# Performance work log

Measured on AMD Instinct MI355X. Metric: run time of the kernel, lower is better.

Reference implementation:

```python
import jax, jax.numpy as jnp
import numpy as np

EPS = 0.01      # label smoothing eps
LAM = 0.5       # SuperLoss lam
ALPHA = 0.25    # FocalLoss alpha
GAMMA = 2.0     # FocalLoss gamma


def lambertw_principal(y, iters=20):
    """Real principal-branch Lambert W for y >= -1/e, via Halley iterations.
    Replaces the scipy.special.lambertw CPU round-trip with on-device math."""
    y = jnp.maximum(y, -jnp.exp(-1.0) + 1e-7)  # clamp to domain of W0
    # init: branch-point series near -1/e, log1p-based elsewhere
    p = jnp.sqrt(2.0 * (jnp.e * y + 1.0))
    w_bp = -1.0 + p - p * p / 3.0
    w = jnp.where(y < 0.0, w_bp, jnp.log1p(y))

    def body(w, _):
        ew = jnp.exp(w)
        f = w * ew - y
        w1 = w + 1.0
        w_next = w - f / (ew * w1 - (w + 2.0) * f / (2.0 * w1))
        return w_next, None

    w, _ = jax.lax.scan(body, w, None, length=iters)
    return w


def setup_inputs() -> dict:
    key = jax.random.key(0)
    k1, k2 = jax.random.split(key)
    B, C = 2048, 50257
    output = jax.random.normal(k1, (B, C), dtype=jnp.float32)
    target = jax.random.randint(k2, (B,), 0, C, dtype=jnp.int64)
    return {"output": output, "target": target}


def reference(output, target):
    B, c = output.shape
    # label-smoothing uniform term: mean over batch of -sum(log_softmax)
    log_preds = jax.nn.log_softmax(output, axis=-1)          # [B, C]
    loss = (-log_preds.sum(axis=-1)).mean()                  # scalar

    # FocalLoss(Superloss=True) applied to log_preds (CE re-applies log_softmax,
    # idempotent on log_preds but kept for fidelity)
    lp2 = jax.nn.log_softmax(log_preds, axis=-1)
    ce = -jnp.take_along_axis(lp2, target[:, None], axis=-1)[:, 0]  # [B]
    pt = jnp.exp(-ce)
    focal = ALPHA * (1.0 - pt) ** GAMMA * ce                 # [B]

    # SuperLoss: sigma computed from detached loss (stop_gradient)
    tau = jnp.log(jnp.float32(c))                            # C == classes
    l_det = jax.lax.stop_gradient(focal)
    cl_score = l_det - tau
    y_ = 0.5 * jnp.maximum(-2.0 / jnp.e, cl_score / LAM)
    sigma = jnp.exp(-lambertw_principal(y_))                 # [B]
    sl = (focal - tau) * sigma + LAM * jnp.log(sigma) ** 2
    sl_mean = sl.mean()

    loss_cls = loss * EPS / c + (1.0 - EPS) * sl_mean
    return loss_cls, jnp.exp(sl_mean)
```

## Files before the change

### kernel.cpp

```cpp
#include <hip/hip_runtime.h>
#include <hip/hip_bf16.h>
#include <math.h>


#define EPS_LS 0.01
#define LAM 0.5
#define ALPHA 0.25

typedef float vf4 __attribute__((ext_vector_type(4)));

__global__ __launch_bounds__(256) void
row_kernel(const float* __restrict__ x, float4* __restrict__ ws, int C) {
    const int row = blockIdx.x;
    const int tid = threadIdx.x;
    const float* xr = x + (size_t)row * (size_t)C;

    float s0 = 0.0f, s1 = 0.0f, s2 = 0.0f, s3 = 0.0f;
    float t0 = 0.0f, t1 = 0.0f, t2 = 0.0f, t3 = 0.0f;

    const int mis = (int)(((size_t)row * (size_t)C) & 3);
    const int pre = (4 - mis) & 3;
    if (tid < pre) {
        float v = xr[tid];
        s0 = __expf(v); t0 = v;
    }
    const int nvec = (C - pre) >> 2;
    const vf4* xv = reinterpret_cast<const vf4*>(xr + pre);

    int i = tid;
    for (; i + 768 < nvec; i += 1024) {
        vf4 v0 = __builtin_nontemporal_load(&xv[i]);
        vf4 v1 = __builtin_nontemporal_load(&xv[i + 256]);
        vf4 v2 = __builtin_nontemporal_load(&xv[i + 512]);
        vf4 v3 = __builtin_nontemporal_load(&xv[i + 768]);
        s0 += (__expf(v0.x) + __expf(v0.y)) + (__expf(v0.z) + __expf(v0.w));
        t0 += (v0.x + v0.y) + (v0.z + v0.w);
        s1 += (__expf(v1.x) + __expf(v1.y)) + (__expf(v1.z) + __expf(v1.w));
        t1 += (v1.x + v1.y) + (v1.z + v1.w);
        s2 += (__expf(v2.x) + __expf(v2.y)) + (__expf(v2.z) + __expf(v2.w));
        t2 += (v2.x + v2.y) + (v2.z + v2.w);
        s3 += (__expf(v3.x) + __expf(v3.y)) + (__expf(v3.z) + __expf(v3.w));
        t3 += (v3.x + v3.y) + (v3.z + v3.w);
    }
    for (; i < nvec; i += 256) {
        vf4 v0 = __builtin_nontemporal_load(&xv[i]);
        s0 += (__expf(v0.x) + __expf(v0.y)) + (__expf(v0.z) + __expf(v0.w));
        t0 += (v0.x + v0.y) + (v0.z + v0.w);
    }
    const int done = pre + (nvec << 2);
    const int rem = C - done;
    if (tid < rem) {
        float v = xr[done + tid];
        s0 += __expf(v); t0 += v;
    }

    float S = (s0 + s1) + (s2 + s3);
    float T = (t0 + t1) + (t2 + t3);

    for (int off = 32; off > 0; off >>= 1) {
        S += __shfl_down(S, off, 64);
        T += __shfl_down(T, off, 64);
    }

    __shared__ float sh_s[4], sh_t[4];
    const int wave = tid >> 6, lane = tid & 63;
    if (lane == 0) { sh_s[wave] = S; sh_t[wave] = T; }
    __syncthreads();

    if (tid == 0) {
        float Sa = ((sh_s[0] + sh_s[1]) + (sh_s[2] + sh_s[3]));
        float Ta = ((sh_t[0] + sh_t[1]) + (sh_t[2] + sh_t[3]));
        ws[row] = make_float4(0.0f, Sa, Ta, 0.0f);
    }
}

__global__ __launch_bounds__(256) void
mid_kernel(const float4* __restrict__ ws, const float* __restrict__ x,
           const int* __restrict__ tgt, double2* __restrict__ part,
           int B, int C) {
    __shared__ double shA[256], shB[256];
    const int tid = threadIdx.x;
    const int row = blockIdx.x * 256 + tid;
    const double tau = log((double)C);
    const double Econst = 2.718281828459045235360287;

    double sl = 0.0, loss = 0.0;
    if (row < B) {
        float4 r = ws[row];
        const double M = (double)r.x;
        const double lse = log((double)r.y);
        const double SX = (double)r.z;
        const double xt = (double)x[(size_t)row * (size_t)C + tgt[row]];
        const double ce = M + lse - xt;
        const double pt = exp(-ce);
        const double omp = 1.0 - pt;
        const double focal = ALPHA * omp * omp * ce;
        const double cl = focal - tau;
        double y_ = 0.5 * fmax(-2.0 / Econst, cl / LAM);
        double y  = fmax(y_, -exp(-1.0) + 1e-7);
        double p  = sqrt(2.0 * (Econst * y + 1.0));
        double w  = (y < 0.0) ? (-1.0 + p - p * p / 3.0) : log1p(y);
        for (int it = 0; it < 20; ++it) {
            double ew = exp(w);
            double f  = w * ew - y;
            double w1 = w + 1.0;
            w = w - f / (ew * w1 - (w + 2.0) * f / (2.0 * w1));
        }
        const double sigma = exp(-w);
        const double lw = log(sigma);
        sl   = cl * sigma + LAM * lw * lw;
        loss = (double)C * (M + lse) - SX;
    }
    shA[tid] = sl; shB[tid] = loss;
    __syncthreads();
    for (int off = 128; off > 0; off >>= 1) {
        if (tid < off) { shA[tid] += shA[tid + off]; shB[tid] += shB[tid + off]; }
        __syncthreads();
    }
    if (tid == 0) part[blockIdx.x] = make_double2(shA[0], shB[0]);
}

__global__ void
final_kernel(const double2* __restrict__ part, float* __restrict__ out,
             int npart, int B, int C) {
    if (threadIdx.x != 0) return;
    double sl_sum = 0.0, loss_sum = 0.0;
    for (int i = 0; i < npart; ++i) { sl_sum += part[i].x; loss_sum += part[i].y; }
    const double sl_mean = sl_sum / (double)B;
    const double loss    = loss_sum / (double)B;
    const double loss_cls = loss * (EPS_LS / (double)C) + (1.0 - EPS_LS) * sl_mean;
    out[0] = (float)loss_cls;
    out[1] = (float)exp(sl_mean);
}

extern "C" void kernel_launch(void* const* d_in, const int* in_sizes, int n_in,
                              void* d_out, int out_size, void* d_ws, size_t ws_size,
                              hipStream_t stream) {
    const float* x   = (const float*)d_in[0];
    const int*   tgt = (const int*)d_in[1];
    float* out = (float*)d_out;
    float4* ws = (float4*)d_ws;

    const int B = in_sizes[1];
    const int C = in_sizes[0] / B;

    const int nmid = (B + 255) / 256;
    double2* part = reinterpret_cast<double2*>((char*)d_ws + (size_t)B * 16);

    row_kernel<<<B, 256, 0, stream>>>(x, ws, C);
    mid_kernel<<<nmid, 256, 0, stream>>>(ws, x, tgt, part, B, C);
    final_kernel<<<1, 64, 0, stream>>>(part, out, nmid, B, C);
}
```

Measured before the change: 492.0 us.

## Fuse row, per-row loss and final reduction into one kernel via last-block counter

```diff
diff --git a/kernel.cpp b/kernel.cpp
--- a/kernel.cpp
+++ b/kernel.cpp
@@ -9,11 +9,20 @@
 
 typedef float vf4 __attribute__((ext_vector_type(4)));
 
+__global__ void init_kernel(unsigned int* __restrict__ counter) {
+    *counter = 0u;
+}
+
 __global__ __launch_bounds__(256) void
-row_kernel(const float* __restrict__ x, float4* __restrict__ ws, int C) {
+fused_kernel(const float* __restrict__ x, const int* __restrict__ tgt,
+             double2* __restrict__ part, unsigned int* __restrict__ counter,
+             float* __restrict__ out, int B, int C) {
     const int row = blockIdx.x;
     const int tid = threadIdx.x;
     const float* xr = x + (size_t)row * (size_t)C;
+
+    float xt_f = 0.0f;
+    if (tid == 0) xt_f = xr[tgt[row]];
 
     float s0 = 0.0f, s1 = 0.0f, s2 = 0.0f, s3 = 0.0f;
     float t0 = 0.0f, t1 = 0.0f, t2 = 0.0f, t3 = 0.0f;
@@ -67,30 +76,17 @@
     if (lane == 0) { sh_s[wave] = S; sh_t[wave] = T; }
     __syncthreads();
 
+    __shared__ unsigned int lastflag;
     if (tid == 0) {
-        float Sa = ((sh_s[0] + sh_s[1]) + (sh_s[2] + sh_s[3]));
-        float Ta = ((sh_t[0] + sh_t[1]) + (sh_t[2] + sh_t[3]));
-        ws[row] = make_float4(0.0f, Sa, Ta, 0.0f);
-    }
-}
+        const float Sa = ((sh_s[0] + sh_s[1]) + (sh_s[2] + sh_s[3]));
+        const float Ta = ((sh_t[0] + sh_t[1]) + (sh_t[2] + sh_t[3]));
 
-__global__ __launch_bounds__(256) void
-mid_kernel(const float4* __restrict__ ws, const float* __restrict__ x,
-           const int* __restrict__ tgt, double2* __restrict__ part,
-           int B, int C) {
-    __shared__ double shA[256], shB[256];
-    const int tid = threadIdx.x;
-    const int row = blockIdx.x * 256 + tid;
-    const double tau = log((double)C);
-    const double Econst = 2.718281828459045235360287;
-
-    double sl = 0.0, loss = 0.0;
-    if (row < B) {
-        float4 r = ws[row];
-        const double M = (double)r.x;
-        const double lse = log((double)r.y);
-        const double SX = (double)r.z;
-        const double xt = (double)x[(size_t)row * (size_t)C + tgt[row]];
+        const double tau = log((double)C);
+        const double Econst = 2.718281828459045235360287;
+        const double M = 0.0;
+        const double lse = log((double)Sa);
+        const double SX = (double)Ta;
+        const double xt = (double)xt_f;
         const double ce = M + lse - xt;
         const double pt = exp(-ce);
         const double omp = 1.0 - pt;
@@ -108,29 +104,38 @@
         }
         const double sigma = exp(-w);
         const double lw = log(sigma);
-        sl   = cl * sigma + LAM * lw * lw;
-        loss = (double)C * (M + lse) - SX;
+        const double sl   = cl * sigma + LAM * lw * lw;
+        const double loss = (double)C * (M + lse) - SX;
+
+        part[row] = make_double2(sl, loss);
+        __threadfence();
+        unsigned int old = atomicAdd(counter, 1u);
+        lastflag = (old == (unsigned int)gridDim.x - 1u) ? 1u : 0u;
     }
-    shA[tid] = sl; shB[tid] = loss;
     __syncthreads();
-    for (int off = 128; off > 0; off >>= 1) {
-        if (tid < off) { shA[tid] += shA[tid + off]; shB[tid] += shB[tid + off]; }
+
+    if (lastflag) {
+        __threadfence();
+        __shared__ double shA[256], shB[256];
+        double a = 0.0, b = 0.0;
+        for (int r = tid; r < B; r += 256) {
+            double2 pr = part[r];
+            a += pr.x; b += pr.y;
+        }
+        shA[tid] = a; shB[tid] = b;
         __syncthreads();
+        for (int off = 128; off > 0; off >>= 1) {
+            if (tid < off) { shA[tid] += shA[tid + off]; shB[tid] += shB[tid + off]; }
+            __syncthreads();
+        }
+        if (tid == 0) {
+            const double sl_mean = shA[0] / (double)B;
+            const double loss    = shB[0] / (double)B;
+            const double loss_cls = loss * (EPS_LS / (double)C) + (1.0 - EPS_LS) * sl_mean;
+            out[0] = (float)loss_cls;
+            out[1] = (float)exp(sl_mean);
+        }
     }
-    if (tid == 0) part[blockIdx.x] = make_double2(shA[0], shB[0]);
-}
-
-__global__ void
-final_kernel(const double2* __restrict__ part, float* __restrict__ out,
-             int npart, int B, int C) {
-    if (threadIdx.x != 0) return;
-    double sl_sum = 0.0, loss_sum = 0.0;
-    for (int i = 0; i < npart; ++i) { sl_sum += part[i].x; loss_sum += part[i].y; }
-    const double sl_mean = sl_sum / (double)B;
-    const double loss    = loss_sum / (double)B;
-    const double loss_cls = loss * (EPS_LS / (double)C) + (1.0 - EPS_LS) * sl_mean;
-    out[0] = (float)loss_cls;
-    out[1] = (float)exp(sl_mean);
 }
 
 extern "C" void kernel_launch(void* const* d_in, const int* in_sizes, int n_in,
@@ -139,15 +144,13 @@
     const float* x   = (const float*)d_in[0];
     const int*   tgt = (const int*)d_in[1];
     float* out = (float*)d_out;
-    float4* ws = (float4*)d_ws;
 
     const int B = in_sizes[1];
     const int C = in_sizes[0] / B;
 
-    const int nmid = (B + 255) / 256;
-    double2* part = reinterpret_cast<double2*>((char*)d_ws + (size_t)B * 16);
+    double2* part = (double2*)d_ws;
+    unsigned int* counter = (unsigned int*)((char*)d_ws + (size_t)B * sizeof(double2));
 
-    row_kernel<<<B, 256, 0, stream>>>(x, ws, C);
-    mid_kernel<<<nmid, 256, 0, stream>>>(ws, x, tgt, part, B, C);
-    final_kernel<<<1, 64, 0, stream>>>(part, out, nmid, B, C);
+    init_kernel<<<1, 1, 0, stream>>>(counter);
+    fused_kernel<<<B, 256, 0, stream>>>(x, tgt, part, counter, out, B, C);
 }
```

New measurement: 600.5 us. 1.22x slower.
